# Kernel tuning notes

Measured on AMD Instinct MI355X. Metric: run time of the kernel, lower is better.

Reference implementation:

```python
import jax, jax.numpy as jnp
import numpy as np

H, DI, N, K, R, FF = 2048, 4096, 16, 4, 128, 5632
B, S = 2, 1024
EPS = 1e-6


def rmsnorm(x, w):
    v = jnp.mean(x * x, axis=-1, keepdims=True)
    return x * jax.lax.rsqrt(v + EPS) * w


def setup_inputs() -> dict:
    key = jax.random.key(0)
    ks = jax.random.split(key, 16)
    sc = 0.02
    inp = {
        "hidden_states": jax.random.normal(ks[0], (B, S, H), jnp.float32),
        "input_ln_w": jnp.ones((H,), jnp.float32),
        "w_in": jax.random.normal(ks[1], (2 * DI, H), jnp.float32) * sc,
        "conv_w": jax.random.normal(ks[2], (DI, 1, K), jnp.float32) * 0.3,
        "conv_b": jax.random.normal(ks[3], (DI,), jnp.float32) * sc,
        "w_x": jax.random.normal(ks[4], (R + 2 * N, DI), jnp.float32) * sc,
        "dt_ln_w": jnp.ones((R,), jnp.float32),
        "b_ln_w": jnp.ones((N,), jnp.float32),
        "c_ln_w": jnp.ones((N,), jnp.float32),
        "w_dt": jax.random.normal(ks[5], (DI, R), jnp.float32) * sc,
        "b_dt": jax.random.normal(ks[6], (DI,), jnp.float32) * sc - 4.0,
        "A_log": jnp.broadcast_to(jnp.log(jnp.arange(1, N + 1, dtype=jnp.float32)), (DI, N)),
        "D_skip": jnp.ones((DI,), jnp.float32),
        "w_out": jax.random.normal(ks[7], (H, DI), jnp.float32) * sc,
        "pre_ff_ln_w": jnp.ones((H,), jnp.float32),
        "w_gate": jax.random.normal(ks[8], (FF, H), jnp.float32) * sc,
        "w_up": jax.random.normal(ks[9], (FF, H), jnp.float32) * sc,
        "w_down": jax.random.normal(ks[10], (H, FF), jnp.float32) * sc,
    }
    return inp


def causal_conv1d(x, w, b):
    # x: [B,S,DI], w: [DI,1,K] depthwise, left-pad K-1 (causal)
    y = jax.lax.conv_general_dilated(
        x.transpose(0, 2, 1), w,
        window_strides=(1,), padding=[(K - 1, 0)],
        dimension_numbers=("NCH", "OIH", "NCH"),
        feature_group_count=DI)
    return (y + b[None, :, None]).transpose(0, 2, 1)


def selective_scan(u, A, Bm, Cm, Dp, dt):
    # u,dt: [B,S,DI]; A: [DI,N]; Bm,Cm: [B,S,N]
    def step(h, xs):
        dt_t, B_t, C_t, u_t = xs  # [B,DI],[B,N],[B,N],[B,DI]
        dA = jnp.exp(dt_t[:, :, None] * A)                      # [B,DI,N]
        dBu = dt_t[:, :, None] * B_t[:, None, :] * u_t[:, :, None]
        h = dA * h + dBu
        y = jnp.einsum("bdn,bn->bd", h, C_t)
        return h, y

    xs = (dt.transpose(1, 0, 2), Bm.transpose(1, 0, 2),
          Cm.transpose(1, 0, 2), u.transpose(1, 0, 2))
    h0 = jnp.zeros((u.shape[0], DI, N), u.dtype)
    _, ys = jax.lax.scan(step, h0, xs)
    return ys.transpose(1, 0, 2) + u * Dp  # [B,S,DI]


def reference(hidden_states, input_ln_w, w_in, conv_w, conv_b, w_x, dt_ln_w,
              b_ln_w, c_ln_w, w_dt, b_dt, A_log, D_skip, w_out, pre_ff_ln_w,
              w_gate, w_up, w_down):
    residual = hidden_states
    x = rmsnorm(hidden_states, input_ln_w)

    # --- Mamba mixer ---
    proj = x @ w_in.T                       # [B,S,2*DI]
    u, gate = jnp.split(proj, 2, axis=-1)
    u = jax.nn.silu(causal_conv1d(u, conv_w, conv_b))
    ssm_p = u @ w_x.T                       # [B,S,R+2N]
    t_r, Bm, Cm = jnp.split(ssm_p, [R, R + N], axis=-1)
    t_r = rmsnorm(t_r, dt_ln_w)
    Bm = rmsnorm(Bm, b_ln_w)
    Cm = rmsnorm(Cm, c_ln_w)
    dt = jax.nn.softplus(t_r @ w_dt.T + b_dt)  # [B,S,DI]
    A = -jnp.exp(A_log)
    y = selective_scan(u, A, Bm, Cm, D_skip, dt)
    y = y * jax.nn.silu(gate)
    mixer_out = y @ w_out.T                  # [B,S,H]

    hidden = residual + mixer_out
    residual = hidden
    h = rmsnorm(hidden, pre_ff_ln_w)
    ff = (jax.nn.silu(h @ w_gate.T) * (h @ w_up.T)) @ w_down.T
    return residual + ff
```

## Files before the change

kernel.cpp:

```cpp
#include <hip/hip_runtime.h>
#include <stdint.h>

#define H_   2048
#define DI_  4096
#define N_   16
#define K_   4
#define R_   128
#define FF_  5632
#define B_   2
#define S_   1024
#define MROWS (B_*S_)
#define PCH  32
#define CSTEPS (S_/PCH)

typedef float f32x4 __attribute__((ext_vector_type(4)));
typedef float f32x2 __attribute__((ext_vector_type(2)));
typedef __bf16 bf16x8 __attribute__((ext_vector_type(8)));

#define LOG2E 1.4426950408889634f
#define LN2   0.6931471805599453f

__device__ __forceinline__ unsigned short f2bf(float f) {
    union { float f; unsigned u; } v; v.f = f;
    unsigned r = v.u + 0x7fffu + ((v.u >> 16) & 1u);
    return (unsigned short)(r >> 16);
}

__device__ __forceinline__ float fexp2(float x) { return __builtin_amdgcn_exp2f(x); }
__device__ __forceinline__ float flog2(float x) { return __builtin_amdgcn_logf(x); }

__device__ __forceinline__ float softplus2(float v) {
    return (v > 20.f) ? v : LN2 * flog2(1.f + fexp2(v * LOG2E));
}

__device__ __forceinline__ void gload16(const void* g, void* lds) {
    __builtin_amdgcn_global_load_lds(
        (const __attribute__((address_space(1))) unsigned int*)(uintptr_t)g,
        (__attribute__((address_space(3))) unsigned int*)(unsigned int)(uintptr_t)lds,
        16, 0, 0);
}

__global__ __launch_bounds__(256, 2)
void gemm_bt(const unsigned short* __restrict__ A, const unsigned short* __restrict__ Bt,
             float* __restrict__ C, int M, int N, int K, int Kc)
{
    __shared__ __align__(16) unsigned short As[128 * 64];
    __shared__ __align__(16) unsigned short Bs[128 * 64];
    const int t = threadIdx.x;
    const int l = t & 63;
    const int wv = t >> 6;

    int nwg = gridDim.x * gridDim.y;
    int wg = blockIdx.y * gridDim.x + blockIdx.x;
    if ((nwg & 7) == 0) {
        int q = nwg >> 3;
        wg = (wg & 7) * q + (wg >> 3);
    }
    const int bx = wg % gridDim.x;
    const int by = wg / gridDim.x;
    const long m0 = (long)by * 128;
    const long n0 = (long)bx * 128;
    const int wm = (wv >> 1) * 64;
    const int wn = (wv & 1) * 64;
    const long kstart = (long)blockIdx.z * Kc;
    C += (long)blockIdx.z * M * (long)N;

    f32x4 acc[4][4] = {};

    const int tr = t >> 3;
    const int cs = (t & 7) ^ (tr & 7);
    const unsigned short* gA = A + (m0 + tr) * (long)K + kstart + cs * 8;
    const unsigned short* gB = Bt + (n0 + tr) * (long)K + kstart + cs * 8;
    const unsigned ldsbase = (unsigned)(t & 192) * 16;

    for (int kt = 0; kt < Kc; kt += 64) {
#pragma unroll
        for (int j = 0; j < 4; ++j) {
            gload16(gA + (long)j * 32 * K, (char*)As + j * 4096 + ldsbase);
            gload16(gB + (long)j * 32 * K, (char*)Bs + j * 4096 + ldsbase);
        }
        gA += 64; gB += 64;
        __syncthreads();
#pragma unroll
        for (int k0 = 0; k0 < 2; ++k0) {
            bf16x8 af[4], bfr[4];
#pragma unroll
            for (int i = 0; i < 4; ++i) {
                int rowa = wm + i * 16 + (l & 15);
                int ca = (k0 * 4 + (l >> 4)) ^ (rowa & 7);
                af[i] = *(const bf16x8*)(As + rowa * 64 + ca * 8);
                int rowb = wn + i * 16 + (l & 15);
                int cb = (k0 * 4 + (l >> 4)) ^ (rowb & 7);
                bfr[i] = *(const bf16x8*)(Bs + rowb * 64 + cb * 8);
            }
#pragma unroll
            for (int i = 0; i < 4; ++i)
#pragma unroll
                for (int jn = 0; jn < 4; ++jn)
                    acc[i][jn] = __builtin_amdgcn_mfma_f32_16x16x32_bf16(
                        af[i], bfr[jn], acc[i][jn], 0, 0, 0);
        }
        __syncthreads();
    }

    const int crow = (l >> 4) * 4;
    const int ccol = l & 15;
#pragma unroll
    for (int i = 0; i < 4; ++i) {
#pragma unroll
        for (int jn = 0; jn < 4; ++jn) {
            long row = m0 + wm + i * 16 + crow;
            long col = n0 + wn + jn * 16 + ccol;
            float* cp = C + row * (long)N + col;
#pragma unroll
            for (int q = 0; q < 4; ++q) cp[(long)q * N] = acc[i][jn][q];
        }
    }
}

__global__ __launch_bounds__(512, 1)
void gemm_bt256(const unsigned short* __restrict__ A, const unsigned short* __restrict__ Bt,
                float* __restrict__ C, int M, int N, int K, int Kc)
{
    __shared__ __align__(16) unsigned short As[2][256 * 64];
    __shared__ __align__(16) unsigned short Bs[2][256 * 64];
    const int t = threadIdx.x;
    const int l = t & 63;
    const int wv = t >> 6;
    const int wm = wv >> 2;
    const int wn = wv & 3;

    int nwg = gridDim.x * gridDim.y;
    int wg = blockIdx.y * gridDim.x + blockIdx.x;
    if ((nwg & 7) == 0) {
        int q = nwg >> 3;
        wg = (wg & 7) * q + (wg >> 3);
    }
    const int bx = wg % gridDim.x;
    const int by = wg / gridDim.x;
    const long m0 = (long)by * 256;
    const long n0 = (long)bx * 256;
    const long kstart = (long)blockIdx.z * Kc;
    C += (long)blockIdx.z * M * (long)N;

    f32x4 acc[8][4] = {};

    const int cs = (t & 7) ^ ((t >> 3) & 7);
    const unsigned short* gA = A + (m0 + (t >> 3)) * (long)K + kstart + cs * 8;
    const unsigned short* gB = Bt + (n0 + (t >> 3)) * (long)K + kstart + cs * 8;
    const int NT = Kc >> 6;

#pragma unroll
    for (int i = 0; i < 4; ++i)
        gload16(gA + (long)i * 64 * K, &As[0][t * 8 + i * 4096]);
#pragma unroll
    for (int i = 0; i < 4; ++i)
        gload16(gB + (long)i * 64 * K, &Bs[0][t * 8 + i * 4096]);

    for (int kt = 0; kt < NT; ++kt) {
        const int buf = kt & 1;
        const long koff = (long)((kt + 1 < NT) ? (kt + 1) : kt) * 64;
#pragma unroll
        for (int i = 0; i < 4; ++i)
            gload16(gA + koff + (long)i * 64 * K, &As[buf ^ 1][t * 8 + i * 4096]);
        asm volatile("s_waitcnt vmcnt(4)" ::: "memory");
        __builtin_amdgcn_sched_barrier(0);
        __builtin_amdgcn_s_barrier();
        __builtin_amdgcn_sched_barrier(0);
        {
            bf16x8 af[8], bfr[4];
#pragma unroll
            for (int nf = 0; nf < 4; ++nf) {
                int rowb = wn * 64 + nf * 16 + (l & 15);
                int cb = (l >> 4) ^ (rowb & 7);
                bfr[nf] = *(const bf16x8*)(&Bs[buf][rowb * 64 + cb * 8]);
            }
#pragma unroll
            for (int mf = 0; mf < 8; ++mf) {
                int rowa = wm * 128 + mf * 16 + (l & 15);
                int ca = (l >> 4) ^ (rowa & 7);
                af[mf] = *(const bf16x8*)(&As[buf][rowa * 64 + ca * 8]);
            }
            __builtin_amdgcn_s_setprio(1);
#pragma unroll
            for (int mf = 0; mf < 8; ++mf)
#pragma unroll
                for (int nf = 0; nf < 4; ++nf)
                    acc[mf][nf] = __builtin_amdgcn_mfma_f32_16x16x32_bf16(
                        af[mf], bfr[nf], acc[mf][nf], 0, 0, 0);
            __builtin_amdgcn_s_setprio(0);
        }
        __builtin_amdgcn_sched_barrier(0);
#pragma unroll
        for (int i = 0; i < 4; ++i)
            gload16(gB + koff + (long)i * 64 * K, &Bs[buf ^ 1][t * 8 + i * 4096]);
        {
            bf16x8 af[8], bfr[4];
#pragma unroll
            for (int nf = 0; nf < 4; ++nf) {
                int rowb = wn * 64 + nf * 16 + (l & 15);
                int cb = (4 + (l >> 4)) ^ (rowb & 7);
                bfr[nf] = *(const bf16x8*)(&Bs[buf][rowb * 64 + cb * 8]);
            }
#pragma unroll
            for (int mf = 0; mf < 8; ++mf) {
                int rowa = wm * 128 + mf * 16 + (l & 15);
                int ca = (4 + (l >> 4)) ^ (rowa & 7);
                af[mf] = *(const bf16x8*)(&As[buf][rowa * 64 + ca * 8]);
            }
            __builtin_amdgcn_s_setprio(1);
#pragma unroll
            for (int mf = 0; mf < 8; ++mf)
#pragma unroll
                for (int nf = 0; nf < 4; ++nf)
                    acc[mf][nf] = __builtin_amdgcn_mfma_f32_16x16x32_bf16(
                        af[mf], bfr[nf], acc[mf][nf], 0, 0, 0);
            __builtin_amdgcn_s_setprio(0);
        }
        __builtin_amdgcn_sched_barrier(0);
        __builtin_amdgcn_s_barrier();
        __builtin_amdgcn_sched_barrier(0);
    }

    const int crow = (l >> 4) * 4;
    const int ccol = l & 15;
#pragma unroll
    for (int mf = 0; mf < 8; ++mf) {
#pragma unroll
        for (int nf = 0; nf < 4; ++nf) {
            long row = m0 + wm * 128 + mf * 16 + crow;
            long col = n0 + wn * 64 + nf * 16 + ccol;
            float* cp = C + row * (long)N + col;
#pragma unroll
            for (int q = 0; q < 4; ++q) cp[(long)q * N] = acc[mf][nf][q];
        }
    }
}

__global__ __launch_bounds__(256)
void cvt_bf16(const float* __restrict__ x, unsigned short* __restrict__ y, long n)
{
    long i = ((long)blockIdx.x * 256 + threadIdx.x) * 4;
    if (i >= n) return;
    float4 v = *(const float4*)(x + i);
    ushort4 o;
    o.x = f2bf(v.x); o.y = f2bf(v.y); o.z = f2bf(v.z); o.w = f2bf(v.w);
    *(ushort4*)(y + i) = o;
}

__global__ __launch_bounds__(256)
void cvt_pad_wx(const float* __restrict__ x, unsigned short* __restrict__ y)
{
    long i = ((long)blockIdx.x * 256 + threadIdx.x) * 4;
    int row = (int)(i >> 12);
    ushort4 o;
    if (row < 160) {
        float4 v = *(const float4*)(x + i);
        o.x = f2bf(v.x); o.y = f2bf(v.y); o.z = f2bf(v.z); o.w = f2bf(v.w);
    } else { o.x = 0; o.y = 0; o.z = 0; o.w = 0; }
    *(ushort4*)(y + i) = o;
}

__global__ __launch_bounds__(256)
void rmsnorm_cast(const float* __restrict__ x, const float* __restrict__ w,
                  unsigned short* __restrict__ out)
{
    const long row = blockIdx.x;
    const float* xr = x + row * H_ + threadIdx.x * 8;
    float4 v0 = *(const float4*)xr;
    float4 v1 = *(const float4*)(xr + 4);
    float xv[8] = {v0.x, v0.y, v0.z, v0.w, v1.x, v1.y, v1.z, v1.w};
    float s = 0.f;
#pragma unroll
    for (int j = 0; j < 8; ++j) s += xv[j] * xv[j];
#pragma unroll
    for (int m = 32; m; m >>= 1) s += __shfl_xor(s, m);
    __shared__ float red[4];
    if ((threadIdx.x & 63) == 0) red[threadIdx.x >> 6] = s;
    __syncthreads();
    s = red[0] + red[1] + red[2] + red[3];
    float inv = rsqrtf(s * (1.f / H_) + 1e-6f);
    const float* wr = w + threadIdx.x * 8;
    unsigned short* op = out + row * H_ + threadIdx.x * 8;
    ushort4 o0, o1;
    o0.x = f2bf(xv[0] * inv * wr[0]); o0.y = f2bf(xv[1] * inv * wr[1]);
    o0.z = f2bf(xv[2] * inv * wr[2]); o0.w = f2bf(xv[3] * inv * wr[3]);
    o1.x = f2bf(xv[4] * inv * wr[4]); o1.y = f2bf(xv[5] * inv * wr[5]);
    o1.z = f2bf(xv[6] * inv * wr[6]); o1.w = f2bf(xv[7] * inv * wr[7]);
    *(ushort4*)op = o0;
    *(ushort4*)(op + 4) = o1;
}

__global__ __launch_bounds__(256)
void add_rmsnorm(const float* __restrict__ a, const float* __restrict__ mx,
                 const float* __restrict__ w, float* __restrict__ hid,
                 unsigned short* __restrict__ hb)
{
    const long row = blockIdx.x;
    const long off = row * H_ + threadIdx.x * 8;
    float xv[8];
    {
        float4 a0 = *(const float4*)(a + off);
        float4 a1 = *(const float4*)(a + off + 4);
        xv[0] = a0.x; xv[1] = a0.y; xv[2] = a0.z; xv[3] = a0.w;
        xv[4] = a1.x; xv[5] = a1.y; xv[6] = a1.z; xv[7] = a1.w;
    }
#pragma unroll
    for (int z = 0; z < 4; ++z) {
        const float* mz = mx + (long)z * MROWS * H_ + off;
        float4 b0 = *(const float4*)mz;
        float4 b1 = *(const float4*)(mz + 4);
        xv[0] += b0.x; xv[1] += b0.y; xv[2] += b0.z; xv[3] += b0.w;
        xv[4] += b1.x; xv[5] += b1.y; xv[6] += b1.z; xv[7] += b1.w;
    }
    float s = 0.f;
#pragma unroll
    for (int j = 0; j < 8; ++j) s += xv[j] * xv[j];
#pragma unroll
    for (int m = 32; m; m >>= 1) s += __shfl_xor(s, m);
    __shared__ float red[4];
    if ((threadIdx.x & 63) == 0) red[threadIdx.x >> 6] = s;
    __syncthreads();
    s = red[0] + red[1] + red[2] + red[3];
    float inv = rsqrtf(s * (1.f / H_) + 1e-6f);
    float4 h0, h1;
    h0.x = xv[0]; h0.y = xv[1]; h0.z = xv[2]; h0.w = xv[3];
    h1.x = xv[4]; h1.y = xv[5]; h1.z = xv[6]; h1.w = xv[7];
    *(float4*)(hid + off) = h0;
    *(float4*)(hid + off + 4) = h1;
    const float* wr = w + threadIdx.x * 8;
    ushort4 o0, o1;
    o0.x = f2bf(xv[0] * inv * wr[0]); o0.y = f2bf(xv[1] * inv * wr[1]);
    o0.z = f2bf(xv[2] * inv * wr[2]); o0.w = f2bf(xv[3] * inv * wr[3]);
    o1.x = f2bf(xv[4] * inv * wr[4]); o1.y = f2bf(xv[5] * inv * wr[5]);
    o1.z = f2bf(xv[6] * inv * wr[6]); o1.w = f2bf(xv[7] * inv * wr[7]);
    *(ushort4*)(hb + off) = o0;
    *(ushort4*)(hb + off + 4) = o1;
}

__global__ __launch_bounds__(256)
void conv_silu(const float* __restrict__ proj, const float* __restrict__ cw,
               const float* __restrict__ cb, float* __restrict__ uf,
               unsigned short* __restrict__ ub)
{
    long i = (long)blockIdx.x * 256 + threadIdx.x;
    int d = (int)(i & (DI_ - 1));
    long sd = i >> 12;
    int s = (int)(sd & (S_ - 1));
    long rb = sd * (2 * DI_) + d;
    float w0 = cw[d * 4], w1 = cw[d * 4 + 1], w2 = cw[d * 4 + 2], w3 = cw[d * 4 + 3];
    float acc = cb[d] + w3 * proj[rb];
    if (s >= 1) acc += w2 * proj[rb - 2 * DI_];
    if (s >= 2) acc += w1 * proj[rb - 4 * DI_];
    if (s >= 3) acc += w0 * proj[rb - 6 * DI_];
    float r = acc / (1.f + __expf(-acc));
    uf[i] = r;
    ub[i] = f2bf(r);
}

__global__ __launch_bounds__(256)
void ssm_norms(const float* __restrict__ ssmp, const float* __restrict__ wdt,
               const float* __restrict__ wb, const float* __restrict__ wc,
               unsigned short* __restrict__ trb, float* __restrict__ Bm,
               float* __restrict__ Cm)
{
    const long row = (long)blockIdx.x * 4 + (threadIdx.x >> 6);
    const int l = threadIdx.x & 63;
    float x0 = 0.f, x1 = 0.f, xb = 0.f, xc = 0.f;
#pragma unroll
    for (int z = 0; z < 8; ++z) {
        const float* rp = ssmp + (long)z * (MROWS * 256) + row * 256;
        x0 += rp[l];
        x1 += rp[64 + l];
        xb += rp[128 + (l & 15)];
        xc += rp[144 + (l & 15)];
    }
    float s = x0 * x0 + x1 * x1;
#pragma unroll
    for (int m = 32; m; m >>= 1) s += __shfl_xor(s, m);
    float inv = rsqrtf(s * (1.f / R_) + 1e-6f);
    trb[row * R_ + l] = f2bf(x0 * inv * wdt[l]);
    trb[row * R_ + 64 + l] = f2bf(x1 * inv * wdt[64 + l]);

    float sb = xb * xb, sc = xc * xc;
#pragma unroll
    for (int m = 8; m; m >>= 1) { sb += __shfl_xor(sb, m); sc += __shfl_xor(sc, m); }
    float invb = rsqrtf(sb * (1.f / N_) + 1e-6f);
    float invc = rsqrtf(sc * (1.f / N_) + 1e-6f);
    if (l < 16) {
        Bm[row * N_ + l] = xb * invb * wb[l];
        Cm[row * N_ + l] = xc * invc * wc[l];
    }
}


__global__ __launch_bounds__(256)
void scan_partA(const float* __restrict__ uf, const float* __restrict__ dtraw,
                const float* __restrict__ bdt, const float* __restrict__ Bm,
                const float* __restrict__ A_log,
                float* __restrict__ TRH, float* __restrict__ TRS)
{
    const int w = __builtin_amdgcn_readfirstlane(threadIdx.x >> 6);
    const int l = threadIdx.x & 63;
    const int task = blockIdx.x * 4 + w;
    const int dchunk = task >> 5;
    const int p = task & 31;
    const int gch0 = dchunk * 64;
    const int batch = gch0 >> 12;
    const int d0 = gch0 & (DI_ - 1);
    const int d = d0 + l;
    const long bS = (long)batch * S_;
    const int t0 = p * CSTEPS;

    float Av2[16];
#pragma unroll
    for (int n = 0; n < 16; ++n)
        Av2[n] = -fexp2(A_log[(long)d * N_ + n] * LOG2E) * LOG2E;
    const float bias = bdt[d];

    float h[16];
#pragma unroll
    for (int n = 0; n < 16; ++n) h[n] = 0.f;
    float sdt = 0.f;

    float uN = uf[(bS + t0) * DI_ + d];
    float tN = dtraw[(bS + t0) * DI_ + d];
    float BN[16];
    {
        const float* Bp = Bm + (bS + t0) * N_;
#pragma unroll
        for (int n = 0; n < 16; ++n) BN[n] = Bp[n];
    }

    for (int s = 0; s < CSTEPS; ++s) {
        float uC = uN, tC = tN;
        float BC[16];
#pragma unroll
        for (int n = 0; n < 16; ++n) BC[n] = BN[n];
        if (s + 1 < CSTEPS) {
            long r2 = bS + t0 + s + 1;
            uN = uf[r2 * DI_ + d];
            tN = dtraw[r2 * DI_ + d];
            const float* Bp = Bm + r2 * N_;
#pragma unroll
            for (int n = 0; n < 16; ++n) BN[n] = Bp[n];
        }
        float dt = softplus2(tC + bias);
        float dtu = dt * uC;
        sdt += dt;
#pragma unroll
        for (int n = 0; n < 16; ++n) {
            float e = fexp2(dt * Av2[n]);
            h[n] = fmaf(e, h[n], dtu * BC[n]);
        }
    }
    float* hp = &TRH[(long)(gch0 + l) * (PCH * 16) + p * 16];
#pragma unroll
    for (int n = 0; n < 16; ++n) hp[n] = h[n];
    TRS[(long)(gch0 + l) * PCH + p] = sdt;
}

__global__ __launch_bounds__(256)
void scan_combine(const float* __restrict__ A_log, const float* __restrict__ TRS,
                  float* __restrict__ TRH)
{
    const int tid = blockIdx.x * 256 + threadIdx.x;
    const int gch = tid >> 4, n = tid & 15;
    const int d = gch & (DI_ - 1);
    const float Av = -__expf(A_log[(long)d * N_ + n]);
    const float* sp = TRS + (long)gch * PCH;
    float* hp = TRH + (long)gch * (PCH * 16) + n;
    float h = 0.f;
#pragma unroll
    for (int p = 0; p < PCH; ++p) {
        float hl = hp[p * 16];
        float e = __expf(Av * sp[p]);
        hp[p * 16] = h;
        h = hl + e * h;
    }
}

__global__ __launch_bounds__(256)
void scan_partC(const float* __restrict__ uf, const float* __restrict__ dtraw,
                const float* __restrict__ bdt, const float* __restrict__ Bm,
                const float* __restrict__ Cm, const float* __restrict__ A_log,
                const float* __restrict__ Dskip, const float* __restrict__ proj,
                const float* __restrict__ TRH, unsigned short* __restrict__ yb)
{
    const int w = __builtin_amdgcn_readfirstlane(threadIdx.x >> 6);
    const int l = threadIdx.x & 63;
    const int task = blockIdx.x * 4 + w;
    const int dchunk = task >> 5;
    const int p = task & 31;
    const int gch0 = dchunk * 64;
    const int batch = gch0 >> 12;
    const int d0 = gch0 & (DI_ - 1);
    const int d = d0 + l;
    const long bS = (long)batch * S_;
    const int t0 = p * CSTEPS;

    float Av2[16];
#pragma unroll
    for (int n = 0; n < 16; ++n)
        Av2[n] = -fexp2(A_log[(long)d * N_ + n] * LOG2E) * LOG2E;
    const float bias = bdt[d];
    const float Dv = Dskip[d];

    float h[16];
    {
        const float* hp = &TRH[(long)(gch0 + l) * (PCH * 16) + p * 16];
#pragma unroll
        for (int n = 0; n < 16; ++n) h[n] = hp[n];
    }

    float uN = uf[(bS + t0) * DI_ + d];
    float tN = dtraw[(bS + t0) * DI_ + d];
    float gN = proj[(bS + t0) * (2L * DI_) + DI_ + d];
    float BN[16], CN[16];
    {
        const float* Bp = Bm + (bS + t0) * N_;
        const float* Cp = Cm + (bS + t0) * N_;
#pragma unroll
        for (int n = 0; n < 16; ++n) { BN[n] = Bp[n]; CN[n] = Cp[n]; }
    }

    for (int s = 0; s < CSTEPS; ++s) {
        float uC = uN, tC = tN, gC = gN;
        float BC[16], CC_[16];
#pragma unroll
        for (int n = 0; n < 16; ++n) { BC[n] = BN[n]; CC_[n] = CN[n]; }
        if (s + 1 < CSTEPS) {
            long r2 = bS + t0 + s + 1;
            uN = uf[r2 * DI_ + d];
            tN = dtraw[r2 * DI_ + d];
            gN = proj[r2 * (2L * DI_) + DI_ + d];
            const float* Bp = Bm + r2 * N_;
            const float* Cp = Cm + r2 * N_;
#pragma unroll
            for (int n = 0; n < 16; ++n) { BN[n] = Bp[n]; CN[n] = Cp[n]; }
        }
        float dt = softplus2(tC + bias);
        float dtu = dt * uC;
        float y = uC * Dv;
#pragma unroll
        for (int n = 0; n < 16; ++n) {
            float e = fexp2(dt * Av2[n]);
            h[n] = fmaf(e, h[n], dtu * BC[n]);
            y = fmaf(h[n], CC_[n], y);
        }
        float eg = fexp2(-gC * LOG2E);
        float sl = gC * __builtin_amdgcn_rcpf(1.f + eg);
        yb[(bS + t0 + s) * DI_ + d] = f2bf(y * sl);
    }
}

__global__ __launch_bounds__(256)
void silu_mul(const float* __restrict__ g, const float* __restrict__ u,
              unsigned short* __restrict__ out, long n)
{
    long i = ((long)blockIdx.x * 256 + threadIdx.x) * 4;
    if (i >= n) return;
    float4 gv = *(const float4*)(g + i);
    float4 uv = *(const float4*)(u + i);
    ushort4 o;
    o.x = f2bf(gv.x / (1.f + __expf(-gv.x)) * uv.x);
    o.y = f2bf(gv.y / (1.f + __expf(-gv.y)) * uv.y);
    o.z = f2bf(gv.z / (1.f + __expf(-gv.z)) * uv.z);
    o.w = f2bf(gv.w / (1.f + __expf(-gv.w)) * uv.w);
    *(ushort4*)(out + i) = o;
}

__global__ __launch_bounds__(256)
void final_add(const float* __restrict__ a, const float* __restrict__ b,
               float* __restrict__ y, long n)
{
    long i = ((long)blockIdx.x * 256 + threadIdx.x) * 4;
    if (i >= n) return;
    float4 av = *(const float4*)(a + i);
    float4 o = av;
#pragma unroll
    for (int z = 0; z < 4; ++z) {
        float4 bv = *(const float4*)(b + (long)z * MROWS * H_ + i);
        o.x += bv.x; o.y += bv.y; o.z += bv.z; o.w += bv.w;
    }
    *(float4*)(y + i) = o;
}

extern "C" void kernel_launch(void* const* d_in, const int* in_sizes, int n_in,
                              void* d_out, int out_size, void* d_ws, size_t ws_size,
                              hipStream_t stream)
{
    const float* hs     = (const float*)d_in[0];
    const float* ln_in  = (const float*)d_in[1];
    const float* w_in   = (const float*)d_in[2];
    const float* conv_w = (const float*)d_in[3];
    const float* conv_b = (const float*)d_in[4];
    const float* w_x    = (const float*)d_in[5];
    const float* dt_ln  = (const float*)d_in[6];
    const float* b_ln   = (const float*)d_in[7];
    const float* c_ln   = (const float*)d_in[8];
    const float* w_dt   = (const float*)d_in[9];
    const float* b_dt   = (const float*)d_in[10];
    const float* A_log  = (const float*)d_in[11];
    const float* Dskip  = (const float*)d_in[12];
    const float* w_out  = (const float*)d_in[13];
    const float* ln_ff  = (const float*)d_in[14];
    const float* w_gate = (const float*)d_in[15];
    const float* w_up   = (const float*)d_in[16];
    const float* w_down = (const float*)d_in[17];
    float* out = (float*)d_out;
    char* ws = (char*)d_ws;

    unsigned short* WB    = (unsigned short*)(ws + 0L);
    unsigned short* XB    = (unsigned short*)(ws + 33554432L);
    float*          PROJ  = (float*)(ws + 41943040L);
    float*          MIX   = (float*)(ws + 41943040L);
    float*          GF    = (float*)(ws + 41943040L);
    float*          FFT   = (float*)(ws + 41943040L);
    float*          UF    = (float*)(ws + 109051904L);
    unsigned short* FFACT = (unsigned short*)(ws + 109051904L);
    unsigned short* UB    = (unsigned short*)(ws + 142606336L);
    float*          HID   = (float*)(ws + 142606336L);
    unsigned short* TRB   = (unsigned short*)(ws + 159383552L);
    float*          BM    = (float*)(ws + 159907840L);
    float*          CM    = (float*)(ws + 160038912L);
    float*          TRS   = (float*)(ws + 160169984L);
    float*          SSMP  = (float*)(ws + 161218560L);
    float*          DTRAW = (float*)(ws + 161218560L);
    float*          TRH   = (float*)(ws + 194772992L);
    float*          UPF   = (float*)(ws + 161218560L);
    unsigned short* YB    = (unsigned short*)(ws + 227803136L);
    unsigned short* HB    = XB;

    auto gemm = [&](const unsigned short* A, const unsigned short* Bt, float* C,
                    int M, int N, int K, int kch) {
        dim3 g(N / 128, M / 128, kch);
        gemm_bt<<<g, 256, 0, stream>>>(A, Bt, C, M, N, K, K / kch);
    };
    auto gemm256 = [&](const unsigned short* A, const unsigned short* Bt, float* C,
                       int M, int N, int K, int kch) {
        dim3 g(N / 256, M / 256, kch);
        gemm_bt256<<<g, 512, 0, stream>>>(A, Bt, C, M, N, K, K / kch);
    };
    auto cvt = [&](const float* x, unsigned short* y, long n) {
        cvt_bf16<<<(int)((n / 4 + 255) / 256), 256, 0, stream>>>(x, y, n);
    };

    cvt(w_in, WB, (long)2 * DI_ * H_);
    rmsnorm_cast<<<MROWS, 256, 0, stream>>>(hs, ln_in, XB);
    gemm256(XB, WB, PROJ, MROWS, 2 * DI_, H_, 1);
    conv_silu<<<(MROWS * DI_) / 256, 256, 0, stream>>>(PROJ, conv_w, conv_b, UF, UB);
    cvt_pad_wx<<<(256 * DI_ / 4) / 256, 256, 0, stream>>>(w_x, WB);
    gemm(UB, WB, SSMP, MROWS, 256, DI_, 8);
    ssm_norms<<<MROWS / 4, 256, 0, stream>>>(SSMP, dt_ln, b_ln, c_ln, TRB, BM, CM);
    cvt(w_dt, WB, (long)DI_ * R_);
    gemm(TRB, WB, DTRAW, MROWS, DI_, R_, 1);
    scan_partA<<<(B_ * DI_ / 64) * PCH / 4, 256, 0, stream>>>(UF, DTRAW, b_dt, BM,
                                                              A_log, TRH, TRS);
    scan_combine<<<(B_ * DI_ * N_) / 256, 256, 0, stream>>>(A_log, TRS, TRH);
    scan_partC<<<(B_ * DI_ / 64) * PCH / 4, 256, 0, stream>>>(UF, DTRAW, b_dt, BM, CM,
                                                              A_log, Dskip, PROJ, TRH, YB);
    cvt(w_out, WB, (long)H_ * DI_);
    gemm256(YB, WB, MIX, MROWS, H_, DI_, 4);
    add_rmsnorm<<<MROWS, 256, 0, stream>>>(hs, MIX, ln_ff, HID, HB);
    cvt(w_gate, WB, (long)FF_ * H_);
    gemm256(HB, WB, GF, MROWS, FF_, H_, 1);
    cvt(w_up, WB, (long)FF_ * H_);
    gemm256(HB, WB, UPF, MROWS, FF_, H_, 1);
    silu_mul<<<(int)(((long)MROWS * FF_ / 4 + 255) / 256), 256, 0, stream>>>(
        GF, UPF, FFACT, (long)MROWS * FF_);
    cvt(w_down, WB, (long)H_ * FF_);
    gemm256(FFACT, WB, FFT, MROWS, H_, FF_, 4);
    final_add<<<(int)(((long)MROWS * H_ / 4 + 255) / 256), 256, 0, stream>>>(
        HID, FFT, out, (long)MROWS * H_);
}
```

Before: 538.9 us.

## Restructure bf16 GEMM main loop into quadrant-phased ping-pong with split staging

Rewrites the 256x256 bf16 MFMA GEMM inner loop so each warp computes its 8x4 fragment grid in four quadrant phases. Global-to-LDS loads are split into halves, with each wave loading specific row groups, and are issued between phases, prefetching up to two k-tiles ahead. The goal is to interleave LDS reads, global loads and MFMA bursts more finely, with barriers between phases, so memory latency is hidden and register pressure from holding all A/B fragments is reduced. In exchange it adds more barriers per k-tile and introduces a subtle buffer-reuse ordering: the kt+2 stage is written into the current buffer while later phases still read A from it.

```diff
diff --git a/kernel.cpp b/kernel.cpp
--- a/kernel.cpp
+++ b/kernel.cpp
@@ -142,81 +142,141 @@
     const long n0 = (long)bx * 256;
     const long kstart = (long)blockIdx.z * Kc;
     C += (long)blockIdx.z * M * (long)N;
+    const int NT = Kc >> 6;
 
     f32x4 acc[8][4] = {};
 
-    const int cs = (t & 7) ^ ((t >> 3) & 7);
-    const unsigned short* gA = A + (m0 + (t >> 3)) * (long)K + kstart + cs * 8;
-    const unsigned short* gB = Bt + (n0 + (t >> 3)) * (long)K + kstart + cs * 8;
-    const int NT = Kc >> 6;
-
-#pragma unroll
-    for (int i = 0; i < 4; ++i)
-        gload16(gA + (long)i * 64 * K, &As[0][t * 8 + i * 4096]);
-#pragma unroll
-    for (int i = 0; i < 4; ++i)
-        gload16(gB + (long)i * 64 * K, &Bs[0][t * 8 + i * 4096]);
+    const int ckl = (l & 7) ^ (l >> 3);
+    auto stageA = [&](int kt2, int bufi, int odd) {
+        if ((unsigned)kt2 < (unsigned)NT) {
+            const long koff = kstart + (long)kt2 * 64;
+#pragma unroll
+            for (int j = 0; j < 2; ++j) {
+                const int idx = ((wv & 4) << 2) + ((wv & 3) << 1) + j + (odd ? 8 : 0);
+                const int row = idx * 8 + (l >> 3);
+                gload16(A + (m0 + row) * (long)K + koff + ckl * 8,
+                        &As[bufi][idx * 512 + l * 8]);
+            }
+        }
+    };
+    auto stageB = [&](int kt2, int bufi, int odd) {
+        if ((unsigned)kt2 < (unsigned)NT) {
+            const long koff = kstart + (long)kt2 * 64;
+#pragma unroll
+            for (int j = 0; j < 2; ++j) {
+                const int idx = ((wv >> 1) << 3) + ((wv & 1) << 1) + j + (odd ? 4 : 0);
+                const int row = idx * 8 + (l >> 3);
+                gload16(Bt + (n0 + row) * (long)K + koff + ckl * 8,
+                        &Bs[bufi][idx * 512 + l * 8]);
+            }
+        }
+    };
+
+    stageA(0, 0, 0); stageB(0, 0, 0);
+    stageA(0, 0, 1); stageB(0, 0, 1);
+    stageA(1, 1, 0); stageB(1, 1, 0);
+    asm volatile("s_waitcnt vmcnt(4)" ::: "memory");
+    __builtin_amdgcn_sched_barrier(0);
+    __builtin_amdgcn_s_barrier();
+    __builtin_amdgcn_sched_barrier(0);
 
     for (int kt = 0; kt < NT; ++kt) {
-        const int buf = kt & 1;
-        const long koff = (long)((kt + 1 < NT) ? (kt + 1) : kt) * 64;
-#pragma unroll
-        for (int i = 0; i < 4; ++i)
-            gload16(gA + koff + (long)i * 64 * K, &As[buf ^ 1][t * 8 + i * 4096]);
+        const int buf = kt & 1, obuf = buf ^ 1;
+        bf16x8 af[4][2], b0[2][2], b1[2][2];
+
+#pragma unroll
+        for (int m = 0; m < 4; ++m)
+#pragma unroll
+            for (int ks = 0; ks < 2; ++ks) {
+                int rowa = wm * 128 + m * 16 + (l & 15);
+                int ca = (ks * 4 + (l >> 4)) ^ (rowa & 7);
+                af[m][ks] = *(const bf16x8*)(&As[buf][rowa * 64 + ca * 8]);
+            }
+#pragma unroll
+        for (int n = 0; n < 2; ++n)
+#pragma unroll
+            for (int ks = 0; ks < 2; ++ks) {
+                int rowb = wn * 64 + n * 16 + (l & 15);
+                int cb = (ks * 4 + (l >> 4)) ^ (rowb & 7);
+                b0[n][ks] = *(const bf16x8*)(&Bs[buf][rowb * 64 + cb * 8]);
+            }
+        stageA(kt + 1, obuf, 1); stageB(kt + 1, obuf, 1);
+        __builtin_amdgcn_s_barrier();
+        __builtin_amdgcn_sched_barrier(0);
+        __builtin_amdgcn_s_setprio(1);
+#pragma unroll
+        for (int m = 0; m < 4; ++m)
+#pragma unroll
+            for (int n = 0; n < 2; ++n)
+#pragma unroll
+                for (int ks = 0; ks < 2; ++ks)
+                    acc[m][n] = __builtin_amdgcn_mfma_f32_16x16x32_bf16(
+                        af[m][ks], b0[n][ks], acc[m][n], 0, 0, 0);
+        __builtin_amdgcn_s_setprio(0);
+        __builtin_amdgcn_sched_barrier(0);
+        __builtin_amdgcn_s_barrier();
+        __builtin_amdgcn_sched_barrier(0);
+
+#pragma unroll
+        for (int n = 0; n < 2; ++n)
+#pragma unroll
+            for (int ks = 0; ks < 2; ++ks) {
+                int rowb = wn * 64 + (2 + n) * 16 + (l & 15);
+                int cb = (ks * 4 + (l >> 4)) ^ (rowb & 7);
+                b1[n][ks] = *(const bf16x8*)(&Bs[buf][rowb * 64 + cb * 8]);
+            }
+        stageA(kt + 2, buf, 0); stageB(kt + 2, buf, 0);
+        __builtin_amdgcn_s_barrier();
+        __builtin_amdgcn_sched_barrier(0);
+        __builtin_amdgcn_s_setprio(1);
+#pragma unroll
+        for (int m = 0; m < 4; ++m)
+#pragma unroll
+            for (int n = 0; n < 2; ++n)
+#pragma unroll
+                for (int ks = 0; ks < 2; ++ks)
+                    acc[m][2 + n] = __builtin_amdgcn_mfma_f32_16x16x32_bf16(
+                        af[m][ks], b1[n][ks], acc[m][2 + n], 0, 0, 0);
+        __builtin_amdgcn_s_setprio(0);
+        __builtin_amdgcn_sched_barrier(0);
+        __builtin_amdgcn_s_barrier();
+        __builtin_amdgcn_sched_barrier(0);
+
+#pragma unroll
+        for (int m = 0; m < 4; ++m)
+#pragma unroll
+            for (int ks = 0; ks < 2; ++ks) {
+                int rowa = wm * 128 + 64 + m * 16 + (l & 15);
+                int ca = (ks * 4 + (l >> 4)) ^ (rowa & 7);
+                af[m][ks] = *(const bf16x8*)(&As[buf][rowa * 64 + ca * 8]);
+            }
+        __builtin_amdgcn_s_barrier();
+        __builtin_amdgcn_sched_barrier(0);
+        __builtin_amdgcn_s_setprio(1);
+#pragma unroll
+        for (int m = 0; m < 4; ++m)
+#pragma unroll
+            for (int n = 0; n < 2; ++n)
+#pragma unroll
+                for (int ks = 0; ks < 2; ++ks)
+                    acc[4 + m][2 + n] = __builtin_amdgcn_mfma_f32_16x16x32_bf16(
+                        af[m][ks], b1[n][ks], acc[4 + m][2 + n], 0, 0, 0);
+        __builtin_amdgcn_s_setprio(0);
+        __builtin_amdgcn_sched_barrier(0);
+        __builtin_amdgcn_s_barrier();
+        __builtin_amdgcn_sched_barrier(0);
+
+        __builtin_amdgcn_s_setprio(1);
+#pragma unroll
+        for (int m = 0; m < 4; ++m)
+#pragma unroll
+            for (int n = 0; n < 2; ++n)
+#pragma unroll
+                for (int ks = 0; ks < 2; ++ks)
+                    acc[4 + m][n] = __builtin_amdgcn_mfma_f32_16x16x32_bf16(
+                        af[m][ks], b0[n][ks], acc[4 + m][n], 0, 0, 0);
+        __builtin_amdgcn_s_setprio(0);
         asm volatile("s_waitcnt vmcnt(4)" ::: "memory");
-        __builtin_amdgcn_sched_barrier(0);
-        __builtin_amdgcn_s_barrier();
-        __builtin_amdgcn_sched_barrier(0);
-        {
-            bf16x8 af[8], bfr[4];
-#pragma unroll
-            for (int nf = 0; nf < 4; ++nf) {
-                int rowb = wn * 64 + nf * 16 + (l & 15);
-                int cb = (l >> 4) ^ (rowb & 7);
-                bfr[nf] = *(const bf16x8*)(&Bs[buf][rowb * 64 + cb * 8]);
-            }
-#pragma unroll
-            for (int mf = 0; mf < 8; ++mf) {
-                int rowa = wm * 128 + mf * 16 + (l & 15);
-                int ca = (l >> 4) ^ (rowa & 7);
-                af[mf] = *(const bf16x8*)(&As[buf][rowa * 64 + ca * 8]);
-            }
-            __builtin_amdgcn_s_setprio(1);
-#pragma unroll
-            for (int mf = 0; mf < 8; ++mf)
-#pragma unroll
-                for (int nf = 0; nf < 4; ++nf)
-                    acc[mf][nf] = __builtin_amdgcn_mfma_f32_16x16x32_bf16(
-                        af[mf], bfr[nf], acc[mf][nf], 0, 0, 0);
-            __builtin_amdgcn_s_setprio(0);
-        }
-        __builtin_amdgcn_sched_barrier(0);
-#pragma unroll
-        for (int i = 0; i < 4; ++i)
-            gload16(gB + koff + (long)i * 64 * K, &Bs[buf ^ 1][t * 8 + i * 4096]);
-        {
-            bf16x8 af[8], bfr[4];
-#pragma unroll
-            for (int nf = 0; nf < 4; ++nf) {
-                int rowb = wn * 64 + nf * 16 + (l & 15);
-                int cb = (4 + (l >> 4)) ^ (rowb & 7);
-                bfr[nf] = *(const bf16x8*)(&Bs[buf][rowb * 64 + cb * 8]);
-            }
-#pragma unroll
-            for (int mf = 0; mf < 8; ++mf) {
-                int rowa = wm * 128 + mf * 16 + (l & 15);
-                int ca = (4 + (l >> 4)) ^ (rowa & 7);
-                af[mf] = *(const bf16x8*)(&As[buf][rowa * 64 + ca * 8]);
-            }
-            __builtin_amdgcn_s_setprio(1);
-#pragma unroll
-            for (int mf = 0; mf < 8; ++mf)
-#pragma unroll
-                for (int nf = 0; nf < 4; ++nf)
-                    acc[mf][nf] = __builtin_amdgcn_mfma_f32_16x16x32_bf16(
-                        af[mf], bfr[nf], acc[mf][nf], 0, 0, 0);
-            __builtin_amdgcn_s_setprio(0);
-        }
         __builtin_amdgcn_sched_barrier(0);
         __builtin_amdgcn_s_barrier();
         __builtin_amdgcn_sched_barrier(0);
```

Result: no change. 544.2 us (+1.0%).
